# Optimization experiments

Measured on AMD Instinct MI355X. Metric: run time of the kernel, lower is better.

Reference implementation:

```python
import jax, jax.numpy as jnp
import numpy as np

N_NODES = 50000
N_EDGES = 800000
IN_DIM = 64
HID_DIM = 128
OUT_DIM = 64
BN_EPS = 1e-5


def _glorot(key, shape):
    fan_in, fan_out = shape[0], shape[1]
    lim = (6.0 / (fan_in + fan_out)) ** 0.5
    return jax.random.uniform(key, shape, jnp.float32, -lim, lim)


def setup_inputs() -> dict:
    key = jax.random.key(0)
    ks = jax.random.split(key, 8)
    x = jax.random.normal(ks[0], (N_NODES, IN_DIM), jnp.float32)
    edge_index = jax.random.randint(ks[1], (2, N_EDGES), 0, N_NODES, jnp.int32)
    return {
        "x": x,
        "edge_index": edge_index,
        # SAGEConv1: lin_l (applied to aggregated neighbors, has bias), lin_r (root, no bias)
        "W1l": _glorot(ks[2], (IN_DIM, HID_DIM)),
        "b1": jnp.zeros((HID_DIM,), jnp.float32),
        "W1r": _glorot(ks[3], (IN_DIM, HID_DIM)),
        # BatchNorm1d params
        "gamma": jnp.ones((HID_DIM,), jnp.float32),
        "beta": jnp.zeros((HID_DIM,), jnp.float32),
        # SAGEConv2
        "W2l": _glorot(ks[4], (HID_DIM, OUT_DIM)),
        "b2": jnp.zeros((OUT_DIM,), jnp.float32),
        "W2r": _glorot(ks[5], (HID_DIM, OUT_DIM)),
    }


def _sage_conv(h, src, dst, Wl, b, Wr, deg_inv):
    # mean-aggregate neighbor features per destination node
    agg = jax.ops.segment_sum(h[src], dst, num_segments=N_NODES)  # [N, d]
    agg = agg * deg_inv[:, None]
    return agg @ Wl + b + h @ Wr


def reference(x, edge_index, W1l, b1, W1r, gamma, beta, W2l, b2, W2r):
    src, dst = edge_index[0], edge_index[1]
    deg = jax.ops.segment_sum(jnp.ones((N_EDGES,), jnp.float32), dst,
                              num_segments=N_NODES)
    deg_inv = jnp.where(deg > 0, 1.0 / jnp.maximum(deg, 1.0), 0.0)

    h = _sage_conv(x, src, dst, W1l, b1, W1r, deg_inv)  # [N, hid]
    # BatchNorm1d (training mode: batch stats over nodes, biased variance)
    mu = jnp.mean(h, axis=0)
    var = jnp.mean((h - mu) ** 2, axis=0)
    h = (h - mu) * jax.lax.rsqrt(var + BN_EPS) * gamma + beta
    h = jax.nn.relu(h)
    out = _sage_conv(h, src, dst, W2l, b2, W2r, deg_inv)  # [N, out]
    return out
```

## Files before the change

kernel.cpp:

```cpp
#include <hip/hip_runtime.h>

#define NN 50000
#define NE 800000
#define HID 128
#define OUTD 64
#define NBK 782
#define BWID 64
#define CAP 1264
#define TILE_E 4096
#define XB 3125
#define HB 196

typedef __attribute__((ext_vector_type(8))) short bf16x8;
typedef __attribute__((ext_vector_type(4))) float f32x4;

static __device__ __forceinline__ unsigned short f2bf(float f) {
    unsigned u = __float_as_uint(f);
    unsigned r = (u + 0x7FFFu + ((u >> 16) & 1u)) >> 16;
    return (unsigned short)r;
}
static __device__ __forceinline__ float bflo(unsigned u) { return __uint_as_float(u << 16); }
static __device__ __forceinline__ float bfhi(unsigned u) { return __uint_as_float(u & 0xffff0000u); }

__global__ __launch_bounds__(256) void prep_bin_kernel(
    const float* __restrict__ x, unsigned short* __restrict__ A1,
    const float* __restrict__ W1l, const float* __restrict__ W1r,
    const float* __restrict__ W2l, const float* __restrict__ W2r,
    unsigned short* __restrict__ BT1, unsigned short* __restrict__ BT2,
    const int* __restrict__ src, const int* __restrict__ dst,
    int* __restrict__ gcur, int2* __restrict__ pairs)
{
    __shared__ int lcnt[NBK];
    __shared__ int lbase[NBK];
    int blk = blockIdx.x, tid = threadIdx.x;
    if (blk >= HB) {
        int b2 = blk - HB;
        if (b2 < XB) {
            int idx = b2 * 256 + tid;
            int n = idx >> 4, q = idx & 15;
            float4 v = ((const float4*)x)[idx];
            ushort4 o;
            o.x = f2bf(v.x); o.y = f2bf(v.y); o.z = f2bf(v.z); o.w = f2bf(v.w);
            *(ushort4*)(A1 + (size_t)n * 128 + 64 + q * 4) = o;
        } else {
            int idx = (b2 - XB) * 256 + tid;
            int j = idx >> 7, k = idx & 127;
            float v1 = (k < 64) ? W1l[k * HID + j] : W1r[(k - 64) * HID + j];
            BT1[j * 128 + k] = f2bf(v1);
            float v2 = (j < 64) ? W2l[k * OUTD + j] : W2r[k * OUTD + (j - 64)];
            BT2[j * 128 + k] = f2bf(v2);
        }
        return;
    }
    int e0 = blk * TILE_E;
    for (int i = tid; i < NBK; i += 256) lcnt[i] = 0;
    __syncthreads();
    int s[16], d[16], loc[16];
#pragma unroll
    for (int i = 0; i < 16; i++) {
        int e = e0 + i * 256 + tid;
        if (e < NE) {
            s[i] = __builtin_nontemporal_load(&src[e]);
            d[i] = __builtin_nontemporal_load(&dst[e]);
            loc[i] = atomicAdd(&lcnt[d[i] >> 6], 1);
        }
    }
    __syncthreads();
    for (int b = tid; b < NBK; b += 256)
        lbase[b] = b * CAP + atomicAdd(&gcur[b], lcnt[b]);
    __syncthreads();
#pragma unroll
    for (int i = 0; i < 16; i++) {
        int e = e0 + i * 256 + tid;
        if (e < NE)
            pairs[lbase[d[i] >> 6] + loc[i]] = make_int2(s[i], d[i]);
    }
}

__global__ __launch_bounds__(256) void binB_kernel(const int2* __restrict__ pairs,
                                                   const int* __restrict__ gcur,
                                                   int* __restrict__ startp,
                                                   int* __restrict__ endp,
                                                   int* __restrict__ perm) {
    __shared__ int lcnt[BWID];
    __shared__ int tmp[256];
    __shared__ int lcur[BWID];
    int b = blockIdx.x, tid = threadIdx.x;
    int lo = b * CAP;
    int hi = lo + gcur[b];
    int base = b * BWID;
    if (tid < BWID) lcnt[tid] = 0;
    __syncthreads();
    for (int i = lo + tid; i < hi; i += 256)
        atomicAdd(&lcnt[pairs[i].y - base], 1);
    __syncthreads();
    int v = (tid < BWID) ? lcnt[tid] : 0;
    tmp[tid] = v;
    __syncthreads();
    for (int off = 1; off < BWID; off <<= 1) {
        int t = (tid >= off) ? tmp[tid - off] : 0;
        __syncthreads();
        tmp[tid] += t;
        __syncthreads();
    }
    if (tid < BWID && base + tid < NN) {
        int s = lo + tmp[tid] - v;
        lcur[tid] = s;
        startp[base + tid] = s;
        endp[base + tid] = s + v;
    }
    __syncthreads();
    for (int i = lo + tid; i < hi; i += 256) {
        int2 p = pairs[i];
        int pos = atomicAdd(&lcur[p.y - base], 1);
        perm[pos] = p.x;
    }
}

template<int MODE>
__global__ __launch_bounds__(256) void agg_gather_b(
    const unsigned short* __restrict__ feat, int fstride, int foff,
    const int* __restrict__ startp, const int* __restrict__ endp,
    const int* __restrict__ perm,
    unsigned short* __restrict__ outb, int ostride, int ooff,
    float* __restrict__ outf)
{
    int wave = (blockIdx.x * blockDim.x + threadIdx.x) >> 6;
    int lane = threadIdx.x & 63;
    int g = lane >> 3;
    int q = lane & 7;
    int node = wave * 8 + g;
    if (node >= NN) return;
    int rs = startp[node];
    int re = endp[node];
    const unsigned short* fbase = feat + foff + q * 8;
    float acc[8];
#pragma unroll
    for (int t = 0; t < 8; t++) acc[t] = 0.f;
    int i = rs;
    for (; i + 1 < re; i += 2) {
        int s0 = perm[i];
        int s1 = perm[i + 1];
        uint4 v0 = *(const uint4*)(fbase + (size_t)s0 * fstride);
        uint4 v1 = *(const uint4*)(fbase + (size_t)s1 * fstride);
        acc[0] += bflo(v0.x); acc[1] += bfhi(v0.x);
        acc[2] += bflo(v0.y); acc[3] += bfhi(v0.y);
        acc[4] += bflo(v0.z); acc[5] += bfhi(v0.z);
        acc[6] += bflo(v0.w); acc[7] += bfhi(v0.w);
        acc[0] += bflo(v1.x); acc[1] += bfhi(v1.x);
        acc[2] += bflo(v1.y); acc[3] += bfhi(v1.y);
        acc[4] += bflo(v1.z); acc[5] += bfhi(v1.z);
        acc[6] += bflo(v1.w); acc[7] += bfhi(v1.w);
    }
    if (i < re) {
        int s0 = perm[i];
        uint4 v0 = *(const uint4*)(fbase + (size_t)s0 * fstride);
        acc[0] += bflo(v0.x); acc[1] += bfhi(v0.x);
        acc[2] += bflo(v0.y); acc[3] += bfhi(v0.y);
        acc[4] += bflo(v0.z); acc[5] += bfhi(v0.z);
        acc[6] += bflo(v0.w); acc[7] += bfhi(v0.w);
    }
    int cnt = re - rs;
    float inv = (cnt > 0) ? (1.0f / (float)cnt) : 0.f;
    if (MODE == 0) {
        uint4 o;
        o.x = (unsigned)f2bf(acc[0] * inv) | ((unsigned)f2bf(acc[1] * inv) << 16);
        o.y = (unsigned)f2bf(acc[2] * inv) | ((unsigned)f2bf(acc[3] * inv) << 16);
        o.z = (unsigned)f2bf(acc[4] * inv) | ((unsigned)f2bf(acc[5] * inv) << 16);
        o.w = (unsigned)f2bf(acc[6] * inv) | ((unsigned)f2bf(acc[7] * inv) << 16);
        *(uint4*)(outb + (size_t)node * ostride + ooff + q * 8) = o;
    } else {
        float4* op = (float4*)(outf + (size_t)node * 64 + q * 8);
        float4 o0 = op[0], o1 = op[1];
        o0.x += acc[0] * inv; o0.y += acc[1] * inv;
        o0.z += acc[2] * inv; o0.w += acc[3] * inv;
        o1.x += acc[4] * inv; o1.y += acc[5] * inv;
        o1.z += acc[6] * inv; o1.w += acc[7] * inv;
        op[0] = o0; op[1] = o1;
    }
}

template<bool IS1>
__global__ __launch_bounds__(256) void conv_mfma_kernel(
    const unsigned short* __restrict__ A, const unsigned short* __restrict__ BT,
    const float* __restrict__ bias,
    unsigned short* __restrict__ outb, float* __restrict__ outf,
    float* __restrict__ sums, float* __restrict__ sumsq)
{
    __shared__ float red_s[4][128];
    __shared__ float red_q[4][128];
    int tid = threadIdx.x;
    int wid = tid >> 6, lane = tid & 63;
    int nl = lane & 15, ko = lane >> 4;
    int gw = blockIdx.x * 4 + wid;
    int jh = gw & 1;
    int tstride = (gridDim.x * 4) >> 1;
    const int tiles = NN / 16;
    bf16x8 b[4][4];
    const unsigned short* bbase = BT + (size_t)(jh * 64 + nl) * 128 + ko * 8;
#pragma unroll
    for (int jg = 0; jg < 4; jg++)
#pragma unroll
        for (int ks = 0; ks < 4; ks++)
            b[jg][ks] = *(const bf16x8*)(bbase + jg * 16 * 128 + ks * 32);
    float4 bias4[4];
#pragma unroll
    for (int jg = 0; jg < 4; jg++) {
        if (IS1)        bias4[jg] = *(const float4*)(bias + jh * 64 + jg * 16 + ko * 4);
        else if (jh)    bias4[jg] = *(const float4*)(bias + jg * 16 + ko * 4);
        else            bias4[jg] = make_float4(0.f, 0.f, 0.f, 0.f);
    }
    float s_sum[16], s_sq[16];
#pragma unroll
    for (int t = 0; t < 16; t++) { s_sum[t] = 0.f; s_sq[t] = 0.f; }
    int tile = gw >> 1;
    bf16x8 a[4];
    if (tile < tiles) {
        const unsigned short* arow = A + (size_t)(tile * 16 + nl) * 128 + ko * 8;
#pragma unroll
        for (int ks = 0; ks < 4; ks++) a[ks] = *(const bf16x8*)(arow + ks * 32);
    }
    while (tile < tiles) {
        int nxt = tile + tstride;
        bf16x8 an[4];
        if (nxt < tiles) {
            const unsigned short* arow = A + (size_t)(nxt * 16 + nl) * 128 + ko * 8;
#pragma unroll
            for (int ks = 0; ks < 4; ks++) an[ks] = *(const bf16x8*)(arow + ks * 32);
        }
        int n_g = tile * 16 + nl;
#pragma unroll
        for (int jg = 0; jg < 4; jg++) {
            f32x4 acc = {0.f, 0.f, 0.f, 0.f};
#pragma unroll
            for (int ks = 0; ks < 4; ks++)
                acc = __builtin_amdgcn_mfma_f32_16x16x32_bf16(b[jg][ks], a[ks], acc, 0, 0, 0);
            float v0 = acc[0] + bias4[jg].x;
            float v1 = acc[1] + bias4[jg].y;
            float v2 = acc[2] + bias4[jg].z;
            float v3 = acc[3] + bias4[jg].w;
            if (IS1) {
                s_sum[jg * 4 + 0] += v0; s_sq[jg * 4 + 0] += v0 * v0;
                s_sum[jg * 4 + 1] += v1; s_sq[jg * 4 + 1] += v1 * v1;
                s_sum[jg * 4 + 2] += v2; s_sq[jg * 4 + 2] += v2 * v2;
                s_sum[jg * 4 + 3] += v3; s_sq[jg * 4 + 3] += v3 * v3;
                uint2 pk;
                pk.x = (unsigned)f2bf(v0) | ((unsigned)f2bf(v1) << 16);
                pk.y = (unsigned)f2bf(v2) | ((unsigned)f2bf(v3) << 16);
                *(uint2*)(outb + (size_t)n_g * 128 + jh * 64 + jg * 16 + ko * 4) = pk;
            } else {
                if (jh == 0) {
                    uint2 pk;
                    pk.x = (unsigned)f2bf(v0) | ((unsigned)f2bf(v1) << 16);
                    pk.y = (unsigned)f2bf(v2) | ((unsigned)f2bf(v3) << 16);
                    *(uint2*)(outb + (size_t)n_g * 64 + jg * 16 + ko * 4) = pk;
                } else {
                    float4 o = make_float4(v0, v1, v2, v3);
                    *(float4*)(outf + (size_t)n_g * 64 + jg * 16 + ko * 4) = o;
                }
            }
        }
#pragma unroll
        for (int ks = 0; ks < 4; ks++) a[ks] = an[ks];
        tile = nxt;
    }
    if (IS1) {
        for (int i = tid; i < 512; i += 256) {
            ((float*)red_s)[i] = 0.f;
            ((float*)red_q)[i] = 0.f;
        }
        __syncthreads();
#pragma unroll
        for (int jg = 0; jg < 4; jg++) {
#pragma unroll
            for (int r = 0; r < 4; r++) {
                float v = s_sum[jg * 4 + r];
                v += __shfl_xor(v, 1, 64);
                v += __shfl_xor(v, 2, 64);
                v += __shfl_xor(v, 4, 64);
                v += __shfl_xor(v, 8, 64);
                float w = s_sq[jg * 4 + r];
                w += __shfl_xor(w, 1, 64);
                w += __shfl_xor(w, 2, 64);
                w += __shfl_xor(w, 4, 64);
                w += __shfl_xor(w, 8, 64);
                if (nl == 0) {
                    red_s[wid][jh * 64 + jg * 16 + ko * 4 + r] = v;
                    red_q[wid][jh * 64 + jg * 16 + ko * 4 + r] = w;
                }
            }
        }
        __syncthreads();
        if (tid < 128) {
            float v = red_s[0][tid] + red_s[1][tid] + red_s[2][tid] + red_s[3][tid];
            atomicAdd(&sums[tid], v);
        } else {
            int j = tid - 128;
            float v = red_q[0][j] + red_q[1][j] + red_q[2][j] + red_q[3][j];
            atomicAdd(&sumsq[j], v);
        }
    }
}

__global__ __launch_bounds__(256) void bnapply_kernel(
    const unsigned short* __restrict__ hpreb,
    const float* __restrict__ sums, const float* __restrict__ sumsq,
    const float* __restrict__ gamma, const float* __restrict__ beta,
    unsigned short* __restrict__ A1)
{
    __shared__ float sc[128], sh[128];
    int tid = threadIdx.x;
    if (tid < 128) {
        float inv_n = 1.0f / (float)NN;
        float mu = sums[tid] * inv_n;
        float var = sumsq[tid] * inv_n - mu * mu;
        float s = gamma[tid] * rsqrtf(var + 1e-5f);
        sc[tid] = s;
        sh[tid] = beta[tid] - mu * s;
    }
    __syncthreads();
    int idx = blockIdx.x * 256 + tid;
    if (idx >= NN * 16) return;
    int q = idx & 15;
    int j0 = q * 8;
    uint4 v = ((const uint4*)hpreb)[idx];
    float f[8];
    f[0] = bflo(v.x); f[1] = bfhi(v.x);
    f[2] = bflo(v.y); f[3] = bfhi(v.y);
    f[4] = bflo(v.z); f[5] = bfhi(v.z);
    f[6] = bflo(v.w); f[7] = bfhi(v.w);
#pragma unroll
    for (int t = 0; t < 8; t++) {
        float h = f[t] * sc[j0 + t] + sh[j0 + t];
        f[t] = h > 0.f ? h : 0.f;
    }
    uint4 o;
    o.x = (unsigned)f2bf(f[0]) | ((unsigned)f2bf(f[1]) << 16);
    o.y = (unsigned)f2bf(f[2]) | ((unsigned)f2bf(f[3]) << 16);
    o.z = (unsigned)f2bf(f[4]) | ((unsigned)f2bf(f[5]) << 16);
    o.w = (unsigned)f2bf(f[6]) | ((unsigned)f2bf(f[7]) << 16);
    ((uint4*)A1)[idx] = o;
}

extern "C" void kernel_launch(void* const* d_in, const int* in_sizes, int n_in,
                              void* d_out, int out_size, void* d_ws, size_t ws_size,
                              hipStream_t stream) {
    const float* x     = (const float*)d_in[0];
    const int*   ei    = (const int*)d_in[1];
    const float* W1l   = (const float*)d_in[2];
    const float* b1    = (const float*)d_in[3];
    const float* W1r   = (const float*)d_in[4];
    const float* gamma = (const float*)d_in[5];
    const float* beta  = (const float*)d_in[6];
    const float* W2l   = (const float*)d_in[7];
    const float* b2    = (const float*)d_in[8];
    const float* W2r   = (const float*)d_in[9];
    float* out = (float*)d_out;

    char* wsb = (char*)d_ws;
    int*   gcur   = (int*)wsb;
    float* sums   = (float*)(wsb + 784 * 4);
    float* sumsq  = sums + 128;
    int*   startp = (int*)(sumsq + 128);
    int*   endp   = startp + NN;
    int*   perm   = endp + NN;
    unsigned short* A1    = (unsigned short*)(perm + NBK * CAP);
    unsigned short* hpreb = A1 + (size_t)NN * 128;
    unsigned short* BT1   = hpreb + (size_t)NN * 128;
    unsigned short* BT2   = BT1 + 128 * 128;
    int2*  pairs  = (int2*)hpreb;

    const int* srcp = ei;
    const int* dstp = ei + NE;

    const int GB = (NN / 8 * 64 + 255) / 256;
    const int CB = 512;

    hipMemsetAsync(d_ws, 0, 784 * 4 + 256 * 4, stream);

    prep_bin_kernel<<<HB + XB + 64, 256, 0, stream>>>(x, A1, W1l, W1r, W2l, W2r,
                                                      BT1, BT2, srcp, dstp, gcur, pairs);
    binB_kernel<<<NBK, 256, 0, stream>>>(pairs, gcur, startp, endp, perm);

    agg_gather_b<0><<<GB, 256, 0, stream>>>(A1, 128, 64, startp, endp, perm,
                                            A1, 128, 0, nullptr);
    conv_mfma_kernel<true><<<CB, 256, 0, stream>>>(A1, BT1, b1, hpreb, nullptr, sums, sumsq);
    bnapply_kernel<<<XB, 256, 0, stream>>>(hpreb, sums, sumsq, gamma, beta, A1);
    conv_mfma_kernel<false><<<CB, 256, 0, stream>>>(A1, BT2, b2, hpreb, out, nullptr, nullptr);
    agg_gather_b<1><<<GB, 256, 0, stream>>>(hpreb, 64, 0, startp, endp, perm,
                                            nullptr, 0, 0, out);
}
```

Measured before the change: 203.5 us.

## Fuse bucket CSR build into aggregation kernels using shared-memory permutation

Removes the separate binB kernel and the global startp/endp/perm arrays. Each aggregation block now takes one 64-node destination bucket, builds its local CSR in shared memory with a wave-shuffle scan, and gathers neighbors from it, with the gather unrolled to 4 loads. The binning work is repeated in both aggregation passes, and pairs moves to its own workspace region so it survives hpreb being overwritten. Only 782 blocks of 256 threads run each aggregation, which may lower occupancy compared with the earlier grid.

```diff
diff --git a/kernel.cpp b/kernel.cpp
--- a/kernel.cpp
+++ b/kernel.cpp
@@ -77,106 +77,113 @@
     }
 }
 
-__global__ __launch_bounds__(256) void binB_kernel(const int2* __restrict__ pairs,
-                                                   const int* __restrict__ gcur,
-                                                   int* __restrict__ startp,
-                                                   int* __restrict__ endp,
-                                                   int* __restrict__ perm) {
-    __shared__ int lcnt[BWID];
-    __shared__ int tmp[256];
-    __shared__ int lcur[BWID];
-    int b = blockIdx.x, tid = threadIdx.x;
-    int lo = b * CAP;
-    int hi = lo + gcur[b];
-    int base = b * BWID;
-    if (tid < BWID) lcnt[tid] = 0;
-    __syncthreads();
-    for (int i = lo + tid; i < hi; i += 256)
-        atomicAdd(&lcnt[pairs[i].y - base], 1);
-    __syncthreads();
-    int v = (tid < BWID) ? lcnt[tid] : 0;
-    tmp[tid] = v;
-    __syncthreads();
-    for (int off = 1; off < BWID; off <<= 1) {
-        int t = (tid >= off) ? tmp[tid - off] : 0;
-        __syncthreads();
-        tmp[tid] += t;
-        __syncthreads();
-    }
-    if (tid < BWID && base + tid < NN) {
-        int s = lo + tmp[tid] - v;
-        lcur[tid] = s;
-        startp[base + tid] = s;
-        endp[base + tid] = s + v;
-    }
-    __syncthreads();
-    for (int i = lo + tid; i < hi; i += 256) {
-        int2 p = pairs[i];
-        int pos = atomicAdd(&lcur[p.y - base], 1);
-        perm[pos] = p.x;
-    }
-}
-
 template<int MODE>
-__global__ __launch_bounds__(256) void agg_gather_b(
+__global__ __launch_bounds__(256) void bin_agg_kernel(
+    const int2* __restrict__ pairs, const int* __restrict__ gcur,
     const unsigned short* __restrict__ feat, int fstride, int foff,
-    const int* __restrict__ startp, const int* __restrict__ endp,
-    const int* __restrict__ perm,
     unsigned short* __restrict__ outb, int ostride, int ooff,
     float* __restrict__ outf)
 {
-    int wave = (blockIdx.x * blockDim.x + threadIdx.x) >> 6;
-    int lane = threadIdx.x & 63;
+    __shared__ int lcnt[BWID];
+    __shared__ int startL[BWID];
+    __shared__ int degL[BWID];
+    __shared__ int lcur[BWID];
+    __shared__ int permL[CAP];
+    int b = blockIdx.x, tid = threadIdx.x;
+    int lo = b * CAP;
+    int cnt = gcur[b];
+    int base = b * BWID;
+    if (tid < BWID) lcnt[tid] = 0;
+    __syncthreads();
+    for (int i = tid; i < cnt; i += 256)
+        atomicAdd(&lcnt[pairs[lo + i].y - base], 1);
+    __syncthreads();
+    if (tid < BWID) {
+        int v = lcnt[tid];
+        int s = v;
+#pragma unroll
+        for (int off = 1; off < BWID; off <<= 1) {
+            int t = __shfl_up(s, off, 64);
+            if (tid >= off) s += t;
+        }
+        startL[tid] = s - v;
+        degL[tid] = v;
+        lcur[tid] = s - v;
+    }
+    __syncthreads();
+    for (int i = tid; i < cnt; i += 256) {
+        int2 p = pairs[lo + i];
+        int pos = atomicAdd(&lcur[p.y - base], 1);
+        permL[pos] = p.x;
+    }
+    __syncthreads();
+    int lane = tid & 63, w = tid >> 6;
     int g = lane >> 3;
     int q = lane & 7;
-    int node = wave * 8 + g;
-    if (node >= NN) return;
-    int rs = startp[node];
-    int re = endp[node];
     const unsigned short* fbase = feat + foff + q * 8;
-    float acc[8];
-#pragma unroll
-    for (int t = 0; t < 8; t++) acc[t] = 0.f;
-    int i = rs;
-    for (; i + 1 < re; i += 2) {
-        int s0 = perm[i];
-        int s1 = perm[i + 1];
-        uint4 v0 = *(const uint4*)(fbase + (size_t)s0 * fstride);
-        uint4 v1 = *(const uint4*)(fbase + (size_t)s1 * fstride);
-        acc[0] += bflo(v0.x); acc[1] += bfhi(v0.x);
-        acc[2] += bflo(v0.y); acc[3] += bfhi(v0.y);
-        acc[4] += bflo(v0.z); acc[5] += bfhi(v0.z);
-        acc[6] += bflo(v0.w); acc[7] += bfhi(v0.w);
-        acc[0] += bflo(v1.x); acc[1] += bfhi(v1.x);
-        acc[2] += bflo(v1.y); acc[3] += bfhi(v1.y);
-        acc[4] += bflo(v1.z); acc[5] += bfhi(v1.z);
-        acc[6] += bflo(v1.w); acc[7] += bfhi(v1.w);
-    }
-    if (i < re) {
-        int s0 = perm[i];
-        uint4 v0 = *(const uint4*)(fbase + (size_t)s0 * fstride);
-        acc[0] += bflo(v0.x); acc[1] += bfhi(v0.x);
-        acc[2] += bflo(v0.y); acc[3] += bfhi(v0.y);
-        acc[4] += bflo(v0.z); acc[5] += bfhi(v0.z);
-        acc[6] += bflo(v0.w); acc[7] += bfhi(v0.w);
-    }
-    int cnt = re - rs;
-    float inv = (cnt > 0) ? (1.0f / (float)cnt) : 0.f;
-    if (MODE == 0) {
-        uint4 o;
-        o.x = (unsigned)f2bf(acc[0] * inv) | ((unsigned)f2bf(acc[1] * inv) << 16);
-        o.y = (unsigned)f2bf(acc[2] * inv) | ((unsigned)f2bf(acc[3] * inv) << 16);
-        o.z = (unsigned)f2bf(acc[4] * inv) | ((unsigned)f2bf(acc[5] * inv) << 16);
-        o.w = (unsigned)f2bf(acc[6] * inv) | ((unsigned)f2bf(acc[7] * inv) << 16);
-        *(uint4*)(outb + (size_t)node * ostride + ooff + q * 8) = o;
-    } else {
-        float4* op = (float4*)(outf + (size_t)node * 64 + q * 8);
-        float4 o0 = op[0], o1 = op[1];
-        o0.x += acc[0] * inv; o0.y += acc[1] * inv;
-        o0.z += acc[2] * inv; o0.w += acc[3] * inv;
-        o1.x += acc[4] * inv; o1.y += acc[5] * inv;
-        o1.z += acc[6] * inv; o1.w += acc[7] * inv;
-        op[0] = o0; op[1] = o1;
+#pragma unroll
+    for (int rnd = 0; rnd < 2; rnd++) {
+        int nloc = w * 16 + rnd * 8 + g;
+        int node = base + nloc;
+        int rs = startL[nloc];
+        int deg = degL[nloc];
+        float acc[8];
+#pragma unroll
+        for (int t = 0; t < 8; t++) acc[t] = 0.f;
+        int i = 0;
+        for (; i + 3 < deg; i += 4) {
+            int s0 = permL[rs + i];
+            int s1 = permL[rs + i + 1];
+            int s2 = permL[rs + i + 2];
+            int s3 = permL[rs + i + 3];
+            uint4 v0 = *(const uint4*)(fbase + (size_t)s0 * fstride);
+            uint4 v1 = *(const uint4*)(fbase + (size_t)s1 * fstride);
+            uint4 v2 = *(const uint4*)(fbase + (size_t)s2 * fstride);
+            uint4 v3 = *(const uint4*)(fbase + (size_t)s3 * fstride);
+            acc[0] += bflo(v0.x); acc[1] += bfhi(v0.x);
+            acc[2] += bflo(v0.y); acc[3] += bfhi(v0.y);
+            acc[4] += bflo(v0.z); acc[5] += bfhi(v0.z);
+            acc[6] += bflo(v0.w); acc[7] += bfhi(v0.w);
+            acc[0] += bflo(v1.x); acc[1] += bfhi(v1.x);
+            acc[2] += bflo(v1.y); acc[3] += bfhi(v1.y);
+            acc[4] += bflo(v1.z); acc[5] += bfhi(v1.z);
+            acc[6] += bflo(v1.w); acc[7] += bfhi(v1.w);
+            acc[0] += bflo(v2.x); acc[1] += bfhi(v2.x);
+            acc[2] += bflo(v2.y); acc[3] += bfhi(v2.y);
+            acc[4] += bflo(v2.z); acc[5] += bfhi(v2.z);
+            acc[6] += bflo(v2.w); acc[7] += bfhi(v2.w);
+            acc[0] += bflo(v3.x); acc[1] += bfhi(v3.x);
+            acc[2] += bflo(v3.y); acc[3] += bfhi(v3.y);
+            acc[4] += bflo(v3.z); acc[5] += bfhi(v3.z);
+            acc[6] += bflo(v3.w); acc[7] += bfhi(v3.w);
+        }
+        for (; i < deg; i++) {
+            int s0 = permL[rs + i];
+            uint4 v0 = *(const uint4*)(fbase + (size_t)s0 * fstride);
+            acc[0] += bflo(v0.x); acc[1] += bfhi(v0.x);
+            acc[2] += bflo(v0.y); acc[3] += bfhi(v0.y);
+            acc[4] += bflo(v0.z); acc[5] += bfhi(v0.z);
+            acc[6] += bflo(v0.w); acc[7] += bfhi(v0.w);
+        }
+        if (node < NN) {
+            float inv = (deg > 0) ? (1.0f / (float)deg) : 0.f;
+            if (MODE == 0) {
+                uint4 o;
+                o.x = (unsigned)f2bf(acc[0] * inv) | ((unsigned)f2bf(acc[1] * inv) << 16);
+                o.y = (unsigned)f2bf(acc[2] * inv) | ((unsigned)f2bf(acc[3] * inv) << 16);
+                o.z = (unsigned)f2bf(acc[4] * inv) | ((unsigned)f2bf(acc[5] * inv) << 16);
+                o.w = (unsigned)f2bf(acc[6] * inv) | ((unsigned)f2bf(acc[7] * inv) << 16);
+                *(uint4*)(outb + (size_t)node * ostride + ooff + q * 8) = o;
+            } else {
+                float4* op = (float4*)(outf + (size_t)node * 64 + q * 8);
+                float4 o0 = op[0], o1 = op[1];
+                o0.x += acc[0] * inv; o0.y += acc[1] * inv;
+                o0.z += acc[2] * inv; o0.w += acc[3] * inv;
+                o1.x += acc[4] * inv; o1.y += acc[5] * inv;
+                o1.z += acc[6] * inv; o1.w += acc[7] * inv;
+                op[0] = o0; op[1] = o1;
+            }
+        }
     }
 }
 
@@ -361,32 +368,26 @@
     int*   gcur   = (int*)wsb;
     float* sums   = (float*)(wsb + 784 * 4);
     float* sumsq  = sums + 128;
-    int*   startp = (int*)(sumsq + 128);
-    int*   endp   = startp + NN;
-    int*   perm   = endp + NN;
-    unsigned short* A1    = (unsigned short*)(perm + NBK * CAP);
+    int2*  pairs  = (int2*)(sumsq + 128);
+    unsigned short* A1    = (unsigned short*)(pairs + (size_t)NBK * CAP);
     unsigned short* hpreb = A1 + (size_t)NN * 128;
     unsigned short* BT1   = hpreb + (size_t)NN * 128;
     unsigned short* BT2   = BT1 + 128 * 128;
-    int2*  pairs  = (int2*)hpreb;
 
     const int* srcp = ei;
     const int* dstp = ei + NE;
 
-    const int GB = (NN / 8 * 64 + 255) / 256;
     const int CB = 512;
 
     hipMemsetAsync(d_ws, 0, 784 * 4 + 256 * 4, stream);
 
     prep_bin_kernel<<<HB + XB + 64, 256, 0, stream>>>(x, A1, W1l, W1r, W2l, W2r,
                                                       BT1, BT2, srcp, dstp, gcur, pairs);
-    binB_kernel<<<NBK, 256, 0, stream>>>(pairs, gcur, startp, endp, perm);
-
-    agg_gather_b<0><<<GB, 256, 0, stream>>>(A1, 128, 64, startp, endp, perm,
-                                            A1, 128, 0, nullptr);
+    bin_agg_kernel<0><<<NBK, 256, 0, stream>>>(pairs, gcur, A1, 128, 64,
+                                               A1, 128, 0, nullptr);
     conv_mfma_kernel<true><<<CB, 256, 0, stream>>>(A1, BT1, b1, hpreb, nullptr, sums, sumsq);
     bnapply_kernel<<<XB, 256, 0, stream>>>(hpreb, sums, sumsq, gamma, beta, A1);
     conv_mfma_kernel<false><<<CB, 256, 0, stream>>>(A1, BT2, b2, hpreb, out, nullptr, nullptr);
-    agg_gather_b<1><<<GB, 256, 0, stream>>>(hpreb, 64, 0, startp, endp, perm,
-                                            nullptr, 0, 0, out);
-}
+    bin_agg_kernel<1><<<NBK, 256, 0, stream>>>(pairs, gcur, hpreb, 64, 0,
+                                               nullptr, 0, 0, out);
+}
```

Result: no change. 199.8 us (-1.8%).
